# Kernel optimization log

Hardware: AMD Instinct MI355X
Metric: run time of the kernel (lower is better)

Reference implementation:

```python
import jax, jax.numpy as jnp
import numpy as np

NUM_HEADS = 32
NUM_KV_HEADS = 8
HEAD_DIM = 128
SEQ = 2048
MAX_SLOTS = 4096
SCALE = float(1.0 / np.sqrt(HEAD_DIM))  # attn_scale
G = NUM_HEADS // NUM_KV_HEADS  # num_queries_per_kv


def setup_inputs() -> dict:
    key = jax.random.key(0)
    k1, k2, k3 = jax.random.split(key, 3)
    q = jax.random.normal(k1, (SEQ, NUM_HEADS, HEAD_DIM), dtype=jnp.float32)
    k = jax.random.normal(k2, (SEQ, NUM_KV_HEADS, HEAD_DIM), dtype=jnp.float32)
    v = jax.random.normal(k3, (SEQ, NUM_KV_HEADS, HEAD_DIM), dtype=jnp.float32)
    k_cache = jnp.zeros((MAX_SLOTS, NUM_KV_HEADS, HEAD_DIM), dtype=jnp.float32)
    v_cache = jnp.zeros((MAX_SLOTS, NUM_KV_HEADS, HEAD_DIM), dtype=jnp.float32)
    slot_mapping = jnp.arange(SEQ, dtype=jnp.int64)  # contiguous block_table slots
    return {"q": q, "k": k, "v": v, "k_cache": k_cache, "v_cache": v_cache,
            "slot_mapping": slot_mapping}


def reference(q, k, v, k_cache, v_cache, slot_mapping):
    # prefill: scatter-write new K/V into the paged cache (self.k_cache[slot_mapping] = k)
    kc = k_cache.at[slot_mapping].set(k)
    vc = v_cache.at[slot_mapping].set(v)
    # gather K/V back from the cache via slot mapping (paged gather pattern)
    k_attn = kc[slot_mapping]  # (S, Hkv, D) == k since slots are unique
    v_attn = vc[slot_mapping]
    # GQA: repeat_interleave kv heads to match query heads
    kr = jnp.repeat(k_attn, G, axis=1)  # (S, H, D)
    vr = jnp.repeat(v_attn, G, axis=1)
    # scores: (H, Sq, Sk), naive full materialization as in the original
    scores = jnp.einsum('qhd,khd->hqk', q, kr) * SCALE
    sq, sk = q.shape[0], k_attn.shape[0]
    mask = jnp.tril(jnp.ones((sq, sk), dtype=bool))  # causal (num_query_tokens > 1)
    scores = jnp.where(mask[None, :, :], scores, -jnp.inf)
    weights = jax.nn.softmax(scores, axis=-1)
    out = jnp.einsum('hqk,khd->qhd', weights, vr)  # (S, H, D)
    return out
```

## Files before the change

### kernel.cpp

```cpp
#include <hip/hip_runtime.h>
#include <hip/hip_bf16.h>

#define SEQ 2048
#define QSTR 4096
#define KSTR 1024
#define CSCALE 0.1275174364688796f

typedef __attribute__((ext_vector_type(8)))  short short8;
typedef __attribute__((ext_vector_type(4)))  float f32x4;
typedef __attribute__((ext_vector_type(16))) float f32x16;

union PF8 { unsigned u[4]; short8 s; };

__device__ __forceinline__ unsigned short f2bf(float f) {
    union { __hip_bfloat16 b; unsigned short u; } cv;
    cv.b = __float2bfloat16(f);
    return cv.u;
}

__device__ __forceinline__ void gload16(const unsigned short* g, unsigned short* l) {
    __builtin_amdgcn_global_load_lds(
        (const __attribute__((address_space(1))) void*)g,
        (__attribute__((address_space(3))) void*)l, 16, 0, 0);
}

__global__ void prep_k(const float* __restrict__ Kg, unsigned short* __restrict__ Kb) {
    int gi = blockIdx.x * 256 + threadIdx.x;
    int kv = gi >> 8;
    int rem = gi & 255;
    int hk = rem >> 5;
    int d4 = rem & 31;
    f32x4 k4 = *(const f32x4*)(Kg + ((size_t)kv * 8 + hk) * 128 + 4 * d4);
    ushort4 u = make_ushort4(f2bf(k4[0]), f2bf(k4[1]), f2bf(k4[2]), f2bf(k4[3]));
    *(ushort4*)(Kb + ((size_t)hk * SEQ + kv) * 128 + 4 * d4) = u;
}

__global__ void prep_v(const float* __restrict__ Vg, unsigned short* __restrict__ Vtb) {
    const int hk  = blockIdx.x >> 5;
    const int kvb = blockIdx.x & 31;
    __shared__ unsigned short T[128][72];
    const int t = threadIdx.x;
    #pragma unroll
    for (int i = 0; i < 8; ++i) {
        int idx = t + 256 * i;
        int r = idx >> 5, d4 = idx & 31;
        f32x4 v = *(const f32x4*)(Vg + ((size_t)(kvb * 64 + r) * 8 + hk) * 128 + 4 * d4);
        T[4 * d4 + 0][r] = f2bf(v[0]);
        T[4 * d4 + 1][r] = f2bf(v[1]);
        T[4 * d4 + 2][r] = f2bf(v[2]);
        T[4 * d4 + 3][r] = f2bf(v[3]);
    }
    __syncthreads();
    #pragma unroll
    for (int i = 0; i < 8; ++i) {
        int idx = t + 256 * i;
        int d = idx >> 4, c4 = idx & 15;
        ushort4 u = *(ushort4*)&T[d][4 * c4];
        *(ushort4*)(Vtb + ((size_t)hk * 128 + d) * SEQ + kvb * 64 + 4 * c4) = u;
    }
}

__launch_bounds__(256, 2)
__global__ void attn_fwd(const float* __restrict__ Qg,
                         const unsigned short* __restrict__ Kb,
                         const unsigned short* __restrict__ Vtb,
                         float* __restrict__ Og) {
    const int bid  = blockIdx.x;
    const int gidx = bid >> 5;
    const int qb   = (gidx < 8) ? (15 - gidx) : (gidx - 8);
    const int h    = bid & 31;
    const int hk   = h >> 2;
    const int tid  = threadIdx.x;
    const int w    = tid >> 6;
    const int lane = tid & 63;
    const int q5   = lane & 31;
    const int t5   = lane >> 5;
    const int swz  = lane & 7;

    __shared__ __align__(16) unsigned char smem[67584];
    typedef unsigned short KsT[64][128];
    typedef unsigned short VtT[128][64];
    KsT* Ks = (KsT*)smem;
    VtT* Vt = (VtT*)(smem + 32768);
    float (*Ot)[132] = (float(*)[132])smem;

    const int q0w = qb * 128 + 32 * w;
    const int nt  = 2 * qb + 2;

    short8 qf[8];
    {
        const float* qp = Qg + (size_t)(q0w + q5) * QSTR + h * 128 + 8 * t5;
        #pragma unroll
        for (int st = 0; st < 8; ++st) {
            f32x4 a = *(const f32x4*)(qp + 16 * st);
            f32x4 b = *(const f32x4*)(qp + 16 * st + 4);
            short8 f;
            f[0] = (short)f2bf(a[0] * CSCALE); f[1] = (short)f2bf(a[1] * CSCALE);
            f[2] = (short)f2bf(a[2] * CSCALE); f[3] = (short)f2bf(a[3] * CSCALE);
            f[4] = (short)f2bf(b[0] * CSCALE); f[5] = (short)f2bf(b[1] * CSCALE);
            f[6] = (short)f2bf(b[2] * CSCALE); f[7] = (short)f2bf(b[3] * CSCALE);
            qf[st] = f;
        }
    }
    #pragma unroll
    for (int st = 0; st < 8; ++st) asm volatile("" :: "v"(qf[st]));
    asm volatile("s_waitcnt vmcnt(0)" ::: "memory");

    f32x16 oacc[4];
    #pragma unroll
    for (int dt = 0; dt < 4; ++dt)
        #pragma unroll
        for (int r = 0; r < 16; ++r) oacc[dt][r] = 0.f;
    float m = -1e30f, l = 0.f;

    auto ISSUE = [&](int t, int b) {
        const int kv0 = t * 64;
        #pragma unroll
        for (int p = 0; p < 4; ++p) {
            int row = 16 * w + 4 * p + (lane >> 4);
            const unsigned short* g = Kb +
                ((size_t)hk * SEQ + kv0 + row) * 128 + 8 * ((lane & 15) ^ (row & 7));
            gload16(g, &Ks[b][16 * w + 4 * p][0]);
        }
        #pragma unroll
        for (int p = 0; p < 4; ++p) {
            int d = 32 * w + 8 * p + (lane >> 3);
            const unsigned short* g = Vtb +
                ((size_t)hk * 128 + d) * SEQ + kv0 + 8 * ((lane & 7) ^ (d & 7));
            gload16(g, &Vt[b][32 * w + 8 * p][0]);
        }
    };

    ISSUE(0, 0);
    if (nt > 1) ISSUE(1, 1);

    for (int t = 0; t < nt; ++t) {
        const int kv0 = t * 64;
        const int buf = t & 1;
        if (t + 1 < nt) asm volatile("s_waitcnt vmcnt(8)" ::: "memory");
        else            asm volatile("s_waitcnt vmcnt(0)" ::: "memory");
        __builtin_amdgcn_s_barrier();

        const bool active = (kv0 <= q0w + 31);
        if (active) {
            f32x16 sac[2];
            __builtin_amdgcn_s_setprio(1);
            #pragma unroll
            for (int kvs = 0; kvs < 2; ++kvs) {
                f32x16 acc;
                #pragma unroll
                for (int r = 0; r < 16; ++r) acc[r] = 0.f;
                #pragma unroll
                for (int st = 0; st < 8; ++st) {
                    short8 kf = *(const short8*)
                        &Ks[buf][32 * kvs + q5][8 * ((2 * st + t5) ^ swz)];
                    acc = __builtin_amdgcn_mfma_f32_32x32x16_bf16(kf, qf[st], acc, 0, 0, 0);
                }
                sac[kvs] = acc;
            }
            __builtin_amdgcn_s_setprio(0);

            if (kv0 + 63 > q0w) {
                const int qrow = q0w + q5;
                #pragma unroll
                for (int kvs = 0; kvs < 2; ++kvs)
                    #pragma unroll
                    for (int r = 0; r < 16; ++r) {
                        int kv = kv0 + 32 * kvs + (r & 3) + 8 * (r >> 2) + 4 * t5;
                        if (kv > qrow) sac[kvs][r] = -1e30f;
                    }
            }

            float mx = sac[0][0];
            #pragma unroll
            for (int kvs = 0; kvs < 2; ++kvs)
                #pragma unroll
                for (int r = 0; r < 16; ++r) mx = fmaxf(mx, sac[kvs][r]);
            mx = fmaxf(mx, __shfl_xor(mx, 32));

            const bool skip = __all(mx <= m + 11.0f);
            float fac = 1.0f;
            if (!skip) {
                float mn = fmaxf(m, mx);
                fac = exp2f(m - mn);
                m = mn;
            }

            float ps = 0.f;
            #pragma unroll
            for (int kvs = 0; kvs < 2; ++kvs)
                #pragma unroll
                for (int r = 0; r < 16; ++r) {
                    float p = exp2f(sac[kvs][r] - m);
                    sac[kvs][r] = p;
                    ps += p;
                }
            ps += __shfl_xor(ps, 32);
            if (!skip) {
                l = l * fac + ps;
                #pragma unroll
                for (int dt = 0; dt < 4; ++dt)
                    #pragma unroll
                    for (int r = 0; r < 16; ++r) oacc[dt][r] *= fac;
            } else {
                l += ps;
            }

            unsigned pkw[2][8];
            #pragma unroll
            for (int a = 0; a < 2; ++a)
                #pragma unroll
                for (int rp = 0; rp < 8; ++rp)
                    pkw[a][rp] = (unsigned)f2bf(sac[a][2 * rp]) |
                                 ((unsigned)f2bf(sac[a][2 * rp + 1]) << 16);

            unsigned xp[2][8];
            #pragma unroll
            for (int a = 0; a < 2; ++a)
                #pragma unroll
                for (int i = 0; i < 8; ++i)
                    xp[a][i] = (unsigned)__shfl_xor((int)pkw[a][i], 32);

            PF8 pf[4];
            #pragma unroll
            for (int ks = 0; ks < 4; ++ks) {
                const int a = ks >> 1;
                #pragma unroll
                for (int j = 0; j < 4; ++j) {
                    const int ib = (j & 1) + 4 * (ks & 1);
                    const unsigned own_lo = pkw[a][ib];
                    const unsigned own_hi = pkw[a][ib + 2];
                    const unsigned par_lo = xp[a][ib];
                    const unsigned par_hi = xp[a][ib + 2];
                    pf[ks].u[j] = (j < 2) ? (t5 ? par_hi : own_lo)
                                          : (t5 ? own_hi : par_lo);
                }
            }

            __builtin_amdgcn_s_setprio(1);
            #pragma unroll
            for (int dt = 0; dt < 4; ++dt) {
                #pragma unroll
                for (int ks = 0; ks < 4; ++ks) {
                    short8 vf = *(const short8*)
                        &Vt[buf][32 * dt + q5][8 * ((2 * ks + t5) ^ swz)];
                    oacc[dt] = __builtin_amdgcn_mfma_f32_32x32x16_bf16(vf, pf[ks].s, oacc[dt], 0, 0, 0);
                }
            }
            __builtin_amdgcn_s_setprio(0);
        }

        asm volatile("" ::: "memory");
        __builtin_amdgcn_s_barrier();
        if (t + 2 < nt) ISSUE(t + 2, buf);
    }

    asm volatile("" ::: "memory");
    const float rl = 1.0f / l;
    #pragma unroll
    for (int dt = 0; dt < 4; ++dt)
        #pragma unroll
        for (int b = 0; b < 4; ++b) {
            f32x4 v;
            v[0] = oacc[dt][4 * b + 0] * rl;
            v[1] = oacc[dt][4 * b + 1] * rl;
            v[2] = oacc[dt][4 * b + 2] * rl;
            v[3] = oacc[dt][4 * b + 3] * rl;
            *(f32x4*)&Ot[32 * w + q5][32 * dt + 8 * b + 4 * t5] = v;
        }
    __syncthreads();
    {
        const int col4 = (tid & 31) * 4;
        const int r0   = tid >> 5;
        float* ob = Og + (size_t)(qb * 128) * QSTR + h * 128;
        #pragma unroll
        for (int i = 0; i < 16; ++i) {
            int row = 8 * i + r0;
            f32x4 v = *(const f32x4*)&Ot[row][col4];
            *(f32x4*)(ob + (size_t)row * QSTR + col4) = v;
        }
    }
}

extern "C" void kernel_launch(void* const* d_in, const int* in_sizes, int n_in,
                              void* d_out, int out_size, void* d_ws, size_t ws_size,
                              hipStream_t stream) {
    const float* q = (const float*)d_in[0];
    const float* k = (const float*)d_in[1];
    const float* v = (const float*)d_in[2];
    float* out = (float*)d_out;
    unsigned short* Kb  = (unsigned short*)d_ws;
    unsigned short* Vtb = Kb + (size_t)8 * SEQ * 128;
    prep_k<<<dim3(2048), 256, 0, stream>>>(k, Kb);
    prep_v<<<dim3(256), 256, 0, stream>>>(v, Vtb);
    attn_fwd<<<dim3(512), 256, 0, stream>>>(q, Kb, Vtb, out);
}
```

Baseline: 89.37 us.

## Halve attention tiles to 64 queries and 32 KV rows with 2-wave blocks

Splits work into 1024 blocks of 128 threads, each handling 64 query rows and streaming 32-row K/V tiles instead of 128 queries and 64-row tiles. The V tile layout gets a new swizzle to fit a 64x64 LDS buffer, and shared memory drops to 32 KB so more blocks fit per CU. The goal is better load balance and occupancy across the causal triangle on a 256-CU part. In exchange each K/V tile is reused by fewer queries, there are more barriers per unit of work, and the output write-back needs two staged passes.

```diff
diff --git a/kernel.cpp b/kernel.cpp
--- a/kernel.cpp
+++ b/kernel.cpp
@@ -3,7 +3,6 @@
 
 #define SEQ 2048
 #define QSTR 4096
-#define KSTR 1024
 #define CSCALE 0.1275174364688796f
 
 typedef __attribute__((ext_vector_type(8)))  short short8;
@@ -60,16 +59,21 @@
     }
 }
 
-__launch_bounds__(256, 2)
+__launch_bounds__(128, 2)
 __global__ void attn_fwd(const float* __restrict__ Qg,
                          const unsigned short* __restrict__ Kb,
                          const unsigned short* __restrict__ Vtb,
                          float* __restrict__ Og) {
-    const int bid  = blockIdx.x;
-    const int gidx = bid >> 5;
-    const int qb   = (gidx < 8) ? (15 - gidx) : (gidx - 8);
-    const int h    = bid & 31;
-    const int hk   = h >> 2;
+    const int bid = blockIdx.x;
+    const int g   = bid >> 5;
+    const int h   = bid & 31;
+    const int hk  = h >> 2;
+    int qb;
+    if      (g < 8)  qb = 31 - g;
+    else if (g < 16) qb = g - 8;
+    else if (g < 24) qb = 39 - g;
+    else             qb = g - 16;
+
     const int tid  = threadIdx.x;
     const int w    = tid >> 6;
     const int lane = tid & 63;
@@ -77,14 +81,14 @@
     const int t5   = lane >> 5;
     const int swz  = lane & 7;
 
-    __shared__ __align__(16) unsigned char smem[67584];
-    typedef unsigned short KsT[64][128];
-    typedef unsigned short VtT[128][64];
+    __shared__ __align__(16) unsigned char smem[32768];
+    typedef unsigned short KsT[32][128];
+    typedef unsigned short VtT[64][64];
     KsT* Ks = (KsT*)smem;
-    VtT* Vt = (VtT*)(smem + 32768);
+    VtT* Vt = (VtT*)(smem + 16384);
     float (*Ot)[132] = (float(*)[132])smem;
 
-    const int q0w = qb * 128 + 32 * w;
+    const int q0w = qb * 64 + 32 * w;
     const int nt  = 2 * qb + 2;
 
     short8 qf[8];
@@ -114,28 +118,30 @@
     float m = -1e30f, l = 0.f;
 
     auto ISSUE = [&](int t, int b) {
-        const int kv0 = t * 64;
+        const int kv0 = t * 32;
         #pragma unroll
         for (int p = 0; p < 4; ++p) {
             int row = 16 * w + 4 * p + (lane >> 4);
-            const unsigned short* g = Kb +
+            const unsigned short* gp = Kb +
                 ((size_t)hk * SEQ + kv0 + row) * 128 + 8 * ((lane & 15) ^ (row & 7));
-            gload16(g, &Ks[b][16 * w + 4 * p][0]);
+            gload16(gp, &Ks[b][16 * w + 4 * p][0]);
         }
         #pragma unroll
         for (int p = 0; p < 4; ++p) {
-            int d = 32 * w + 8 * p + (lane >> 3);
-            const unsigned short* g = Vtb +
-                ((size_t)hk * 128 + d) * SEQ + kv0 + 8 * ((lane & 7) ^ (d & 7));
-            gload16(g, &Vt[b][32 * w + 8 * p][0]);
+            int d2 = 32 * w + 8 * p + (lane >> 3);
+            int c  = (lane & 7) ^ (d2 & 7);
+            int d  = d2 + 64 * (c >> 2);
+            const unsigned short* gp = Vtb +
+                ((size_t)hk * 128 + d) * SEQ + kv0 + 8 * (c & 3);
+            gload16(gp, &Vt[b][32 * w + 8 * p][0]);
         }
     };
 
     ISSUE(0, 0);
-    if (nt > 1) ISSUE(1, 1);
+    ISSUE(1, 1);
 
     for (int t = 0; t < nt; ++t) {
-        const int kv0 = t * 64;
+        const int kv0 = t * 32;
         const int buf = t & 1;
         if (t + 1 < nt) asm volatile("s_waitcnt vmcnt(8)" ::: "memory");
         else            asm volatile("s_waitcnt vmcnt(0)" ::: "memory");
@@ -143,39 +149,33 @@
 
         const bool active = (kv0 <= q0w + 31);
         if (active) {
-            f32x16 sac[2];
+            f32x16 sac;
+            #pragma unroll
+            for (int r = 0; r < 16; ++r) sac[r] = 0.f;
             __builtin_amdgcn_s_setprio(1);
             #pragma unroll
-            for (int kvs = 0; kvs < 2; ++kvs) {
-                f32x16 acc;
-                #pragma unroll
-                for (int r = 0; r < 16; ++r) acc[r] = 0.f;
-                #pragma unroll
-                for (int st = 0; st < 8; ++st) {
-                    short8 kf = *(const short8*)
-                        &Ks[buf][32 * kvs + q5][8 * ((2 * st + t5) ^ swz)];
-                    acc = __builtin_amdgcn_mfma_f32_32x32x16_bf16(kf, qf[st], acc, 0, 0, 0);
-                }
-                sac[kvs] = acc;
+            for (int st = 0; st < 8; ++st) {
+                short8 kf = *(const short8*)&Ks[buf][q5][8 * ((2 * st + t5) ^ swz)];
+                sac = __builtin_amdgcn_mfma_f32_32x32x16_bf16(kf, qf[st], sac, 0, 0, 0);
             }
             __builtin_amdgcn_s_setprio(0);
 
-            if (kv0 + 63 > q0w) {
+            if (kv0 + 31 > q0w) {
                 const int qrow = q0w + q5;
                 #pragma unroll
-                for (int kvs = 0; kvs < 2; ++kvs)
-                    #pragma unroll
-                    for (int r = 0; r < 16; ++r) {
-                        int kv = kv0 + 32 * kvs + (r & 3) + 8 * (r >> 2) + 4 * t5;
-                        if (kv > qrow) sac[kvs][r] = -1e30f;
-                    }
-            }
-
-            float mx = sac[0][0];
-            #pragma unroll
-            for (int kvs = 0; kvs < 2; ++kvs)
-                #pragma unroll
-                for (int r = 0; r < 16; ++r) mx = fmaxf(mx, sac[kvs][r]);
+                for (int r = 0; r < 16; ++r) {
+                    int kv = kv0 + (r & 3) + 8 * (r >> 2) + 4 * t5;
+                    if (kv > qrow) sac[r] = -1e30f;
+                }
+            }
+
+            float m8[8], m4[4], m2[2];
+            #pragma unroll
+            for (int i = 0; i < 8; ++i) m8[i] = fmaxf(sac[i], sac[i + 8]);
+            #pragma unroll
+            for (int i = 0; i < 4; ++i) m4[i] = fmaxf(m8[i], m8[i + 4]);
+            m2[0] = fmaxf(m4[0], m4[2]); m2[1] = fmaxf(m4[1], m4[3]);
+            float mx = fmaxf(m2[0], m2[1]);
             mx = fmaxf(mx, __shfl_xor(mx, 32));
 
             const bool skip = __all(mx <= m + 11.0f);
@@ -186,15 +186,15 @@
                 m = mn;
             }
 
-            float ps = 0.f;
-            #pragma unroll
-            for (int kvs = 0; kvs < 2; ++kvs)
-                #pragma unroll
-                for (int r = 0; r < 16; ++r) {
-                    float p = exp2f(sac[kvs][r] - m);
-                    sac[kvs][r] = p;
-                    ps += p;
-                }
+            #pragma unroll
+            for (int r = 0; r < 16; ++r) sac[r] = exp2f(sac[r] - m);
+            float s8[8], s4[4], s2[2];
+            #pragma unroll
+            for (int i = 0; i < 8; ++i) s8[i] = sac[i] + sac[i + 8];
+            #pragma unroll
+            for (int i = 0; i < 4; ++i) s4[i] = s8[i] + s8[i + 4];
+            s2[0] = s4[0] + s4[2]; s2[1] = s4[1] + s4[3];
+            float ps = s2[0] + s2[1];
             ps += __shfl_xor(ps, 32);
             if (!skip) {
                 l = l * fac + ps;
@@ -206,32 +206,27 @@
                 l += ps;
             }
 
-            unsigned pkw[2][8];
-            #pragma unroll
-            for (int a = 0; a < 2; ++a)
-                #pragma unroll
-                for (int rp = 0; rp < 8; ++rp)
-                    pkw[a][rp] = (unsigned)f2bf(sac[a][2 * rp]) |
-                                 ((unsigned)f2bf(sac[a][2 * rp + 1]) << 16);
-
-            unsigned xp[2][8];
-            #pragma unroll
-            for (int a = 0; a < 2; ++a)
-                #pragma unroll
-                for (int i = 0; i < 8; ++i)
-                    xp[a][i] = (unsigned)__shfl_xor((int)pkw[a][i], 32);
-
-            PF8 pf[4];
-            #pragma unroll
-            for (int ks = 0; ks < 4; ++ks) {
-                const int a = ks >> 1;
+            unsigned pkw[8];
+            #pragma unroll
+            for (int rp = 0; rp < 8; ++rp)
+                pkw[rp] = (unsigned)f2bf(sac[2 * rp]) |
+                          ((unsigned)f2bf(sac[2 * rp + 1]) << 16);
+
+            unsigned xp[8];
+            #pragma unroll
+            for (int i = 0; i < 8; ++i)
+                xp[i] = (unsigned)__shfl_xor((int)pkw[i], 32);
+
+            PF8 pf[2];
+            #pragma unroll
+            for (int ks = 0; ks < 2; ++ks) {
                 #pragma unroll
                 for (int j = 0; j < 4; ++j) {
-                    const int ib = (j & 1) + 4 * (ks & 1);
-                    const unsigned own_lo = pkw[a][ib];
-                    const unsigned own_hi = pkw[a][ib + 2];
-                    const unsigned par_lo = xp[a][ib];
-                    const unsigned par_hi = xp[a][ib + 2];
+                    const int ib = (j & 1) + 4 * ks;
+                    const unsigned own_lo = pkw[ib];
+                    const unsigned own_hi = pkw[ib + 2];
+                    const unsigned par_lo = xp[ib];
+                    const unsigned par_hi = xp[ib + 2];
                     pf[ks].u[j] = (j < 2) ? (t5 ? par_hi : own_lo)
                                           : (t5 ? own_hi : par_lo);
                 }
@@ -241,9 +236,10 @@
             #pragma unroll
             for (int dt = 0; dt < 4; ++dt) {
                 #pragma unroll
-                for (int ks = 0; ks < 4; ++ks) {
+                for (int ks = 0; ks < 2; ++ks) {
                     short8 vf = *(const short8*)
-                        &Vt[buf][32 * dt + q5][8 * ((2 * ks + t5) ^ swz)];
+                        &Vt[buf][32 * (dt & 1) + q5]
+                           [8 * (((dt >> 1) * 4 + 2 * ks + t5) ^ swz)];
                     oacc[dt] = __builtin_amdgcn_mfma_f32_32x32x16_bf16(vf, pf[ks].s, oacc[dt], 0, 0, 0);
                 }
             }
@@ -258,27 +254,32 @@
     asm volatile("" ::: "memory");
     const float rl = 1.0f / l;
     #pragma unroll
-    for (int dt = 0; dt < 4; ++dt)
-        #pragma unroll
-        for (int b = 0; b < 4; ++b) {
-            f32x4 v;
-            v[0] = oacc[dt][4 * b + 0] * rl;
-            v[1] = oacc[dt][4 * b + 1] * rl;
-            v[2] = oacc[dt][4 * b + 2] * rl;
-            v[3] = oacc[dt][4 * b + 3] * rl;
-            *(f32x4*)&Ot[32 * w + q5][32 * dt + 8 * b + 4 * t5] = v;
-        }
-    __syncthreads();
-    {
-        const int col4 = (tid & 31) * 4;
-        const int r0   = tid >> 5;
-        float* ob = Og + (size_t)(qb * 128) * QSTR + h * 128;
-        #pragma unroll
-        for (int i = 0; i < 16; ++i) {
-            int row = 8 * i + r0;
-            f32x4 v = *(const f32x4*)&Ot[row][col4];
-            *(f32x4*)(ob + (size_t)row * QSTR + col4) = v;
-        }
+    for (int pass = 0; pass < 2; ++pass) {
+        if (w == pass) {
+            #pragma unroll
+            for (int dt = 0; dt < 4; ++dt)
+                #pragma unroll
+                for (int rq = 0; rq < 4; ++rq) {
+                    f32x4 v;
+                    v[0] = oacc[dt][4 * rq + 0] * rl;
+                    v[1] = oacc[dt][4 * rq + 1] * rl;
+                    v[2] = oacc[dt][4 * rq + 2] * rl;
+                    v[3] = oacc[dt][4 * rq + 3] * rl;
+                    *(f32x4*)&Ot[q5][32 * dt + 8 * rq + 4 * t5] = v;
+                }
+        }
+        __syncthreads();
+        {
+            float* ob = Og + (size_t)(qb * 64 + pass * 32) * QSTR + h * 128;
+            #pragma unroll
+            for (int i = 0; i < 8; ++i) {
+                int u = tid + 128 * i;
+                int row = u >> 5, c4 = (u & 31) * 4;
+                f32x4 v = *(const f32x4*)&Ot[row][c4];
+                *(f32x4*)(ob + (size_t)row * QSTR + c4) = v;
+            }
+        }
+        __syncthreads();
     }
 }
 
@@ -293,5 +294,5 @@
     unsigned short* Vtb = Kb + (size_t)8 * SEQ * 128;
     prep_k<<<dim3(2048), 256, 0, stream>>>(k, Kb);
     prep_v<<<dim3(256), 256, 0, stream>>>(v, Vtb);
-    attn_fwd<<<dim3(512), 256, 0, stream>>>(q, Kb, Vtb, out);
-}
+    attn_fwd<<<dim3(1024), 128, 0, stream>>>(q, Kb, Vtb, out);
+}
```

Measured after the change: 101.7 us. 13.8% more time.
